# Performance work log

Measured on AMD Instinct MI355X. Metric: run time of the kernel, lower is better.

## Reference

```python
import jax, jax.numpy as jnp
import numpy as np

E = 23   # unique experts
K = 3    # active experts per token
D = 1024 # in_features
H = 4096 # hidden_features

def setup_inputs() -> dict:
    key = jax.random.key(0)
    ks = jax.random.split(key, 8)
    s = jnp.float32(0.02)
    return {
        "x": jax.random.normal(ks[0], (4, 2048, D), jnp.float32),
        "gate_W": jax.random.normal(ks[1], (D, E), jnp.float32) * s,
        "gate_b": jnp.zeros((E,), jnp.float32),
        "W1": jax.random.normal(ks[2], (E, D, H), jnp.float32) * s,
        "b1": jnp.zeros((E, H), jnp.float32),
        "W2": jax.random.normal(ks[3], (E, H, D), jnp.float32) * s,
        "b2": jnp.zeros((E, D), jnp.float32),
        "sW1": jax.random.normal(ks[4], (D, H), jnp.float32) * s,
        "sb1": jnp.zeros((H,), jnp.float32),
        "sW2": jax.random.normal(ks[5], (H, D), jnp.float32) * s,
        "sb2": jnp.zeros((D,), jnp.float32),
        "bias": jnp.zeros((E,), jnp.float32),  # registered buffer, zeros
    }

def _mlp(x, w1, bb1, w2, bb2):
    # torch nn.GELU default is exact (erf) GELU; drop=0 so dropout is identity
    return jax.nn.gelu(x @ w1 + bb1, approximate=False) @ w2 + bb2

def reference(x, gate_W, gate_b, W1, b1, W2, b2, sW1, sb1, sW2, sb2, bias):
    oshape = x.shape
    xf = x.reshape(-1, oshape[-1])            # [N, D]
    N = xf.shape[0]
    gw = jax.nn.sigmoid(xf @ gate_W + gate_b) # [N, E]
    # top-k selected on (gate + bias), weights gathered from raw gate
    _, topi = jax.lax.top_k(gw + bias, K)     # [N, K]
    topw = jnp.take_along_axis(gw, topi, axis=-1)
    topw = topw / topw.sum(-1, keepdims=True)
    # dense [N, E] combine-weight matrix (0 for unselected experts);
    # per-token topk indices are distinct so .set is safe
    wmat = jnp.zeros((N, E), gw.dtype).at[jnp.arange(N)[:, None], topi].set(topw)
    shared = _mlp(xf, sW1, sb1, sW2, sb2)     # shared expert over all tokens
    # scan over the 23 experts, accumulating weighted expert outputs.
    # (jit-friendly stand-in for the variable-size dispatch/grouped-GEMM.)
    def body(acc, ws):
        w1, bb1, w2, bb2, wcol = ws
        return acc + wcol[:, None] * _mlp(xf, w1, bb1, w2, bb2), None
    out, _ = jax.lax.scan(body, shared, (W1, b1, W2, b2, wmat.T))
    # load-balance auxiliary loss
    counts = jnp.zeros((E,), jnp.float32).at[topi.reshape(-1)].add(1.0)
    P = (gw / gw.sum(-1, keepdims=True)).mean(0)
    Fload = E * counts / (K * N)
    return out.reshape(oshape), (P * Fload).sum()
```

## Files before the change

kernel.cpp:

```cpp
#include <hip/hip_runtime.h>
#include <math.h>

#define DD 1024
#define HH 4096
#define EE 23
#define KK 3
#define NTOK 8192
#define BM 128
#define BN 128
#define BK 32
#define MAXROWS 35712
#define MAXTILES 280

typedef unsigned short u16;
typedef __attribute__((ext_vector_type(8))) short bf16x8;
typedef __attribute__((ext_vector_type(4))) float f32x4;
typedef __attribute__((address_space(3))) unsigned int lds_u32;
typedef const __attribute__((address_space(1))) unsigned int gbl_u32;

struct Tile { int rowStart; int validEnd; int expert; };

__device__ __forceinline__ u16 f2bf(float f) {
    unsigned int u = __float_as_uint(f);
    unsigned int r = 0x7FFFu + ((u >> 16) & 1u);
    return (u16)((u + r) >> 16);
}
__device__ __forceinline__ float gelu_exact(float x) {
    float z = x * 0.70710678118654752f;
    float a = fabsf(z);
    float t = __builtin_amdgcn_rcpf(1.0f + 0.3275911f * a);
    float e = __builtin_amdgcn_exp2f(-a * a * 1.4426950408889634f);
    float p = t * (0.254829592f + t * (-0.284496736f + t * (1.421413741f +
              t * (-1.453152027f + t * 1.061405429f))));
    float er = 1.0f - p * e;
    er = (z < 0.0f) ? -er : er;
    return 0.5f * x * (1.0f + er);
}
__device__ __forceinline__ void gl2lds16(const u16* g, u16* l) {
    __builtin_amdgcn_global_load_lds((gbl_u32*)g, (lds_u32*)l, 16, 0, 0);
}

__global__ void k_convert_x(const float* __restrict__ x, u16* __restrict__ xbf) {
    int i = blockIdx.x * blockDim.x + threadIdx.x;
    float4 v = reinterpret_cast<const float4*>(x)[i];
    ushort4 o;
    o.x = f2bf(v.x); o.y = f2bf(v.y); o.z = f2bf(v.z); o.w = f2bf(v.w);
    reinterpret_cast<ushort4*>(xbf)[i] = o;
}

__global__ void k_transpose(const float* __restrict__ src, u16* __restrict__ dst, int R, int C) {
    __shared__ float tile[64][65];
    size_t base = (size_t)blockIdx.z * R * C;
    src += base; dst += base;
    int ct = blockIdx.x, rt = blockIdx.y, t = threadIdx.x;
    int r0 = rt * 64, c0 = ct * 64;
#pragma unroll
    for (int i = 0; i < 4; i++) {
        int r = i * 16 + (t >> 4);
        int c = (t & 15) * 4;
        float4 v = *reinterpret_cast<const float4*>(&src[(size_t)(r0 + r) * C + c0 + c]);
        tile[r][c] = v.x; tile[r][c + 1] = v.y; tile[r][c + 2] = v.z; tile[r][c + 3] = v.w;
    }
    __syncthreads();
#pragma unroll
    for (int i = 0; i < 4; i++) {
        int c = i * 16 + (t >> 4);
        int r = (t & 15) * 4;
        ushort4 o;
        o.x = f2bf(tile[r][c]);     o.y = f2bf(tile[r + 1][c]);
        o.z = f2bf(tile[r + 2][c]); o.w = f2bf(tile[r + 3][c]);
        *reinterpret_cast<ushort4*>(&dst[(size_t)(c0 + c) * R + r0 + r]) = o;
    }
}

__global__ void k_gate(const float* __restrict__ x, const float* __restrict__ gW,
                       const float* __restrict__ gb, const float* __restrict__ ebias,
                       int* __restrict__ topi, float* __restrict__ topw,
                       int* __restrict__ counts, float* __restrict__ psum) {
    int tok = blockIdx.x, t = threadIdx.x;
    float acc[EE];
#pragma unroll
    for (int e = 0; e < EE; e++) acc[e] = 0.f;
    float4 xv = reinterpret_cast<const float4*>(x + (size_t)tok * DD)[t];
    float xs[4] = {xv.x, xv.y, xv.z, xv.w};
#pragma unroll
    for (int i = 0; i < 4; i++) {
        const float* grow = gW + (size_t)(t * 4 + i) * EE;
        float xd = xs[i];
#pragma unroll
        for (int e = 0; e < EE; e++) acc[e] += xd * grow[e];
    }
#pragma unroll
    for (int e = 0; e < EE; e++) {
        float v = acc[e];
        for (int off = 32; off; off >>= 1) v += __shfl_down(v, off);
        acc[e] = v;
    }
    __shared__ float part[4][EE];
    __shared__ float gwS[EE], scoreS[EE], rowsumS;
    int wave = t >> 6, lane = t & 63;
    if (lane == 0) {
#pragma unroll
        for (int e = 0; e < EE; e++) part[wave][e] = acc[e];
    }
    __syncthreads();
    if (t < EE) {
        float v = part[0][t] + part[1][t] + part[2][t] + part[3][t] + gb[t];
        float g = 1.f / (1.f + expf(-v));
        gwS[t] = g;
        scoreS[t] = g + ebias[t];
    }
    __syncthreads();
    if (t == 0) {
        int i0 = 0, i1 = -1, i2 = -1;
        float s0 = -1e30f, s1 = -1e30f, s2 = -1e30f;
        for (int e = 0; e < EE; e++) {
            float s = scoreS[e];
            if (s > s0)      { s2 = s1; i2 = i1; s1 = s0; i1 = i0; s0 = s; i0 = e; }
            else if (s > s1) { s2 = s1; i2 = i1; s1 = s;  i1 = e; }
            else if (s > s2) { s2 = s;  i2 = e; }
        }
        float w0 = gwS[i0], w1 = gwS[i1], w2 = gwS[i2];
        float wsum = w0 + w1 + w2;
        topi[tok * 3] = i0; topi[tok * 3 + 1] = i1; topi[tok * 3 + 2] = i2;
        topw[tok * 3] = w0 / wsum; topw[tok * 3 + 1] = w1 / wsum; topw[tok * 3 + 2] = w2 / wsum;
        atomicAdd(&counts[i0], 1); atomicAdd(&counts[i1], 1); atomicAdd(&counts[i2], 1);
        float rs = 0.f;
        for (int e = 0; e < EE; e++) rs += gwS[e];
        rowsumS = rs;
    }
    __syncthreads();
    if (t < EE) atomicAdd(&psum[t], gwS[t] / rowsumS);
}

__global__ void k_setup(const int* __restrict__ counts, const float* __restrict__ psum,
                        int* __restrict__ offs, Tile* __restrict__ tiles,
                        int* __restrict__ numTiles, float* __restrict__ out_aux) {
    if (threadIdx.x != 0 || blockIdx.x != 0) return;
    int nt = 0;
    for (int i = 0; i < NTOK / BM; i++) {
        tiles[nt].rowStart = i * BM; tiles[nt].validEnd = NTOK; tiles[nt].expert = EE; nt++;
    }
    int base = NTOK;
    for (int e = 0; e < EE; e++) {
        offs[e] = base;
        int c = counts[e];
        int ntile = (c + BM - 1) / BM;
        for (int i = 0; i < ntile; i++) {
            tiles[nt].rowStart = base + i * BM; tiles[nt].validEnd = base + c; tiles[nt].expert = e; nt++;
        }
        base += ntile * BM;
    }
    numTiles[0] = nt;
    float aux = 0.f;
    for (int e = 0; e < EE; e++)
        aux += (psum[e] / (float)NTOK) * ((float)EE * (float)counts[e] / ((float)KK * (float)NTOK));
    out_aux[0] = aux;
}

__global__ void k_scatter(const int* __restrict__ topi, const float* __restrict__ topw,
                          const int* __restrict__ offs, int* __restrict__ cursor,
                          int* __restrict__ rowTok, float* __restrict__ rowW) {
    int tok = blockIdx.x * blockDim.x + threadIdx.x;
    if (tok >= NTOK) return;
    rowTok[tok] = tok; rowW[tok] = 1.0f;
    for (int k = 0; k < KK; k++) {
        int e = topi[tok * 3 + k];
        int pos = atomicAdd(&cursor[e], 1);
        int slot = offs[e] + pos;
        rowTok[slot] = tok; rowW[slot] = topw[tok * 3 + k];
    }
}

__global__ __launch_bounds__(256) void k_gemm1(
    const u16* __restrict__ xbf, const u16* __restrict__ w1t, const u16* __restrict__ sw1t,
    const float* __restrict__ b1, const float* __restrict__ sb1,
    const int* __restrict__ rowTok, const Tile* __restrict__ tiles,
    const int* __restrict__ numTiles, u16* __restrict__ hbuf, int chunkBase, int hrows) {
    int b = blockIdx.x;
    int xcd = b & 7;
    int j = b >> 3;
    int pb = j / MAXTILES;
    int ti = j - pb * MAXTILES;
    int p  = xcd * 4 + pb;
    if (ti >= numTiles[0]) return;
    Tile tl = tiles[ti];
    if (tl.rowStart < chunkBase || tl.rowStart >= chunkBase + hrows) return;
    int e = tl.expert;
    const u16* wbase = (e == EE) ? sw1t : (w1t + (size_t)e * HH * DD);
    const float* bias = (e == EE) ? sb1 : (b1 + (size_t)e * HH);
    int hbase = p * BN;
    int t = threadIdx.x, lane = t & 63, wv = t >> 6, wr = wv >> 1, wc = wv & 1;

    __shared__ u16 As[BM * BK];
    __shared__ u16 Bs[BN * BK];

    int rbase = wv * 16 + (lane >> 2);
    int c8 = (lane & 3) * 8;
    int s0 = tl.rowStart + rbase, s1 = s0 + 64;
    int tA0 = (s0 < tl.validEnd) ? rowTok[s0] : 0;
    int tA1 = (s1 < tl.validEnd) ? rowTok[s1] : 0;
    const u16* a0 = xbf + (size_t)tA0 * DD + c8;
    const u16* a1 = xbf + (size_t)tA1 * DD + c8;
    const u16* g0 = wbase + (size_t)(hbase + rbase) * DD + c8;
    const u16* g1 = wbase + (size_t)(hbase + 64 + rbase) * DD + c8;
    u16* lA = &As[t * 8];
    u16* lB = &Bs[t * 8];

    f32x4 acc[4][4];
#pragma unroll
    for (int m = 0; m < 4; m++)
#pragma unroll
        for (int n = 0; n < 4; n++) acc[m][n] = (f32x4){0.f, 0.f, 0.f, 0.f};

    for (int kt = 0; kt < DD / BK; kt++) {
        __syncthreads();
        gl2lds16(a0, lA); gl2lds16(a1, lA + 2048);
        gl2lds16(g0, lB); gl2lds16(g1, lB + 2048);
        a0 += BK; a1 += BK; g0 += BK; g1 += BK;
        __syncthreads();
        bf16x8 af[4], bw[4];
#pragma unroll
        for (int m = 0; m < 4; m++)
            af[m] = *reinterpret_cast<const bf16x8*>(&As[(wr * 64 + m * 16 + (lane & 15)) * BK + (lane >> 4) * 8]);
#pragma unroll
        for (int n = 0; n < 4; n++)
            bw[n] = *reinterpret_cast<const bf16x8*>(&Bs[(wc * 64 + n * 16 + (lane & 15)) * BK + (lane >> 4) * 8]);
#pragma unroll
        for (int m = 0; m < 4; m++)
#pragma unroll
            for (int n = 0; n < 4; n++)
                acc[m][n] = __builtin_amdgcn_mfma_f32_16x16x32_bf16(af[m], bw[n], acc[m][n], 0, 0, 0);
    }

#pragma unroll
    for (int m = 0; m < 4; m++) {
        int rowl = wr * 64 + m * 16 + (lane >> 4) * 4;
#pragma unroll
        for (int r = 0; r < 4; r++) {
            int slotr = tl.rowStart + rowl + r;
            bool valid = slotr < tl.validEnd;
            size_t hoff = (size_t)(slotr - chunkBase) * HH;
#pragma unroll
            for (int n = 0; n < 4; n++) {
                int col = hbase + wc * 64 + n * 16 + (lane & 15);
                float v = acc[m][n][r] + bias[col];
                hbuf[hoff + col] = valid ? f2bf(gelu_exact(v)) : (u16)0;
            }
        }
    }
}

__global__ __launch_bounds__(256) void k_gemm2(
    const u16* __restrict__ hbuf, const u16* __restrict__ w2t, const u16* __restrict__ sw2t,
    const float* __restrict__ b2, const float* __restrict__ sb2,
    const int* __restrict__ rowTok, const float* __restrict__ rowW,
    const Tile* __restrict__ tiles, const int* __restrict__ numTiles,
    float* __restrict__ out, int chunkBase, int hrows) {
    const int T = MAXTILES * (DD / BN);
    int b = blockIdx.x;
    int key = (b & 7) * (T >> 3) + (b >> 3);
    int sid = key >> 2, wi = key & 3;
    int ti = (sid >> 2) * 2 + (wi >> 1);
    int p  = ((sid & 3) << 1) + (wi & 1);
    if (ti >= numTiles[0]) return;
    Tile tl = tiles[ti];
    if (tl.rowStart < chunkBase || tl.rowStart >= chunkBase + hrows) return;
    int e = tl.expert;
    const u16* wbase = (e == EE) ? sw2t : (w2t + (size_t)e * DD * HH);
    const float* bias = (e == EE) ? sb2 : (b2 + (size_t)e * DD);
    int dbase = p * BN;
    int t = threadIdx.x, lane = t & 63, wv = t >> 6, wr = wv >> 1, wc = wv & 1;

    __shared__ u16 As[BM * BK];
    __shared__ u16 Bs[BN * BK];

    int rbase = wv * 16 + (lane >> 2);
    int c8 = (lane & 3) * 8;
    const u16* a0 = hbuf + (size_t)(tl.rowStart - chunkBase + rbase) * HH + c8;
    const u16* a1 = hbuf + (size_t)(tl.rowStart - chunkBase + 64 + rbase) * HH + c8;
    const u16* g0 = wbase + (size_t)(dbase + rbase) * HH + c8;
    const u16* g1 = wbase + (size_t)(dbase + 64 + rbase) * HH + c8;
    u16* lA = &As[t * 8];
    u16* lB = &Bs[t * 8];

    f32x4 acc[4][4];
#pragma unroll
    for (int m = 0; m < 4; m++)
#pragma unroll
        for (int n = 0; n < 4; n++) acc[m][n] = (f32x4){0.f, 0.f, 0.f, 0.f};

    for (int kt = 0; kt < HH / BK; kt++) {
        __syncthreads();
        gl2lds16(a0, lA); gl2lds16(a1, lA + 2048);
        gl2lds16(g0, lB); gl2lds16(g1, lB + 2048);
        a0 += BK; a1 += BK; g0 += BK; g1 += BK;
        __syncthreads();
        bf16x8 af[4], bw[4];
#pragma unroll
        for (int m = 0; m < 4; m++)
            af[m] = *reinterpret_cast<const bf16x8*>(&As[(wr * 64 + m * 16 + (lane & 15)) * BK + (lane >> 4) * 8]);
#pragma unroll
        for (int n = 0; n < 4; n++)
            bw[n] = *reinterpret_cast<const bf16x8*>(&Bs[(wc * 64 + n * 16 + (lane & 15)) * BK + (lane >> 4) * 8]);
#pragma unroll
        for (int m = 0; m < 4; m++)
#pragma unroll
            for (int n = 0; n < 4; n++)
                acc[m][n] = __builtin_amdgcn_mfma_f32_16x16x32_bf16(af[m], bw[n], acc[m][n], 0, 0, 0);
    }

#pragma unroll
    for (int m = 0; m < 4; m++) {
        int rowl = wr * 64 + m * 16 + (lane >> 4) * 4;
#pragma unroll
        for (int r = 0; r < 4; r++) {
            int slotr = tl.rowStart + rowl + r;
            if (slotr < tl.validEnd) {
                int tok2 = rowTok[slotr];
                float wgt = rowW[slotr];
                float* orow = out + (size_t)tok2 * DD;
#pragma unroll
                for (int n = 0; n < 4; n++) {
                    int col = dbase + wc * 64 + n * 16 + (lane & 15);
                    float v = acc[m][n][r] + bias[col];
                    atomicAdd(&orow[col], wgt * v);
                }
            }
        }
    }
}

extern "C" void kernel_launch(void* const* d_in, const int* in_sizes, int n_in,
                              void* d_out, int out_size, void* d_ws, size_t ws_size,
                              hipStream_t stream) {
    const float* x    = (const float*)d_in[0];
    const float* gW   = (const float*)d_in[1];
    const float* gb   = (const float*)d_in[2];
    const float* W1   = (const float*)d_in[3];
    const float* b1   = (const float*)d_in[4];
    const float* W2   = (const float*)d_in[5];
    const float* b2   = (const float*)d_in[6];
    const float* sW1  = (const float*)d_in[7];
    const float* sb1  = (const float*)d_in[8];
    const float* sW2  = (const float*)d_in[9];
    const float* sb2  = (const float*)d_in[10];
    const float* ebias = (const float*)d_in[11];
    float* out = (float*)d_out;

    char* w = (char*)d_ws;
    size_t off = 0;
    auto alloc = [&](size_t bytes) -> void* {
        void* p = w + off;
        off += (bytes + 255) & ~(size_t)255;
        return p;
    };
    u16* xbf   = (u16*)alloc((size_t)NTOK * DD * 2);
    u16* w1t   = (u16*)alloc((size_t)EE * HH * DD * 2);
    u16* w2t   = (u16*)alloc((size_t)EE * DD * HH * 2);
    u16* sw1t  = (u16*)alloc((size_t)HH * DD * 2);
    u16* sw2t  = (u16*)alloc((size_t)DD * HH * 2);
    int* topi  = (int*)alloc((size_t)NTOK * 3 * 4);
    float* topw = (float*)alloc((size_t)NTOK * 3 * 4);
    int* counts = (int*)alloc(128);
    float* psum = (float*)alloc(128);
    int* cursor = (int*)alloc(128);
    int* offs   = (int*)alloc(128);
    int* rowTok = (int*)alloc((size_t)MAXROWS * 4);
    float* rowW = (float*)alloc((size_t)MAXROWS * 4);
    Tile* tiles = (Tile*)alloc((size_t)MAXTILES * sizeof(Tile));
    int* numTiles = (int*)alloc(128);

    size_t fixed = off;
    size_t remain = (ws_size > fixed) ? (ws_size - fixed) : 0;
    long hr = (long)(remain / ((size_t)HH * 2));
    if (hr > MAXROWS) hr = MAXROWS;
    hr &= ~(long)127;
    if (hr < 128) hr = 128;
    int hrows = (int)hr;
    int passes = (MAXROWS + hrows - 1) / hrows;
    u16* hbuf = (u16*)(w + fixed);

    hipMemsetAsync(d_out, 0, (size_t)NTOK * DD * 4, stream);
    hipMemsetAsync(counts, 0, 768, stream);

    k_convert_x<<<NTOK, 256, 0, stream>>>(x, xbf);
    k_transpose<<<dim3(HH / 64, DD / 64, EE), 256, 0, stream>>>(W1, w1t, DD, HH);
    k_transpose<<<dim3(DD / 64, HH / 64, EE), 256, 0, stream>>>(W2, w2t, HH, DD);
    k_transpose<<<dim3(HH / 64, DD / 64, 1), 256, 0, stream>>>(sW1, sw1t, DD, HH);
    k_transpose<<<dim3(DD / 64, HH / 64, 1), 256, 0, stream>>>(sW2, sw2t, HH, DD);
    k_gate<<<NTOK, 256, 0, stream>>>(x, gW, gb, ebias, topi, topw, counts, psum);
    k_setup<<<1, 64, 0, stream>>>(counts, psum, offs, tiles, numTiles, out + (size_t)NTOK * DD);
    k_scatter<<<NTOK / 256, 256, 0, stream>>>(topi, topw, offs, cursor, rowTok, rowW);

    for (int p = 0; p < passes; p++) {
        k_gemm1<<<MAXTILES * (HH / BN), 256, 0, stream>>>(
            xbf, w1t, sw1t, b1, sb1, rowTok, tiles, numTiles, hbuf, p * hrows, hrows);
        k_gemm2<<<MAXTILES * (DD / BN), 256, 0, stream>>>(
            hbuf, w2t, sw2t, b2, sb2, rowTok, rowW, tiles, numTiles, out, p * hrows, hrows);
    }
}
```

Baseline: 1.485 ms.

## Double-buffer LDS tiles in both expert GEMMs and regroup gemm1 block mapping

Both grouped GEMM kernels now keep two LDS stages. The next K-slice is issued with direct global-to-LDS loads while the current one is computed, and partial vmcnt waits plus raw barriers replace the two full syncthreads per iteration. gemm1 also swaps its XCD/tile block mapping for a swizzle that groups 8 row tiles by 4 column panels, aiming for better L2 reuse of weights and activations. LDS use doubles, which may cut occupancy, and the hand-written waitcnt counts depend on how gl2lds16 is compiled.

```diff
diff --git a/kernel.cpp b/kernel.cpp
--- a/kernel.cpp
+++ b/kernel.cpp
@@ -177,12 +177,12 @@
     const float* __restrict__ b1, const float* __restrict__ sb1,
     const int* __restrict__ rowTok, const Tile* __restrict__ tiles,
     const int* __restrict__ numTiles, u16* __restrict__ hbuf, int chunkBase, int hrows) {
+    const int T = MAXTILES * (HH / BN);
     int b = blockIdx.x;
-    int xcd = b & 7;
-    int j = b >> 3;
-    int pb = j / MAXTILES;
-    int ti = j - pb * MAXTILES;
-    int p  = xcd * 4 + pb;
+    int key = (b & 7) * (T >> 3) + (b >> 3);
+    int sid = key >> 5, wi = key & 31;
+    int ti = (sid >> 3) * 8 + (wi >> 2);
+    int p  = ((sid & 7) << 2) + (wi & 3);
     if (ti >= numTiles[0]) return;
     Tile tl = tiles[ti];
     if (tl.rowStart < chunkBase || tl.rowStart >= chunkBase + hrows) return;
@@ -192,8 +192,8 @@
     int hbase = p * BN;
     int t = threadIdx.x, lane = t & 63, wv = t >> 6, wr = wv >> 1, wc = wv & 1;
 
-    __shared__ u16 As[BM * BK];
-    __shared__ u16 Bs[BN * BK];
+    __shared__ u16 As[2][BM * BK];
+    __shared__ u16 Bs[2][BN * BK];
 
     int rbase = wv * 16 + (lane >> 2);
     int c8 = (lane & 3) * 8;
@@ -204,8 +204,6 @@
     const u16* a1 = xbf + (size_t)tA1 * DD + c8;
     const u16* g0 = wbase + (size_t)(hbase + rbase) * DD + c8;
     const u16* g1 = wbase + (size_t)(hbase + 64 + rbase) * DD + c8;
-    u16* lA = &As[t * 8];
-    u16* lB = &Bs[t * 8];
 
     f32x4 acc[4][4];
 #pragma unroll
@@ -213,25 +211,41 @@
 #pragma unroll
         for (int n = 0; n < 4; n++) acc[m][n] = (f32x4){0.f, 0.f, 0.f, 0.f};
 
-    for (int kt = 0; kt < DD / BK; kt++) {
-        __syncthreads();
+    auto stage = [&](int buf) {
+        u16* lA = &As[buf][t * 8];
+        u16* lB = &Bs[buf][t * 8];
         gl2lds16(a0, lA); gl2lds16(a1, lA + 2048);
         gl2lds16(g0, lB); gl2lds16(g1, lB + 2048);
         a0 += BK; a1 += BK; g0 += BK; g1 += BK;
-        __syncthreads();
+    };
+    auto compute = [&](int buf) {
         bf16x8 af[4], bw[4];
 #pragma unroll
         for (int m = 0; m < 4; m++)
-            af[m] = *reinterpret_cast<const bf16x8*>(&As[(wr * 64 + m * 16 + (lane & 15)) * BK + (lane >> 4) * 8]);
+            af[m] = *reinterpret_cast<const bf16x8*>(&As[buf][(wr * 64 + m * 16 + (lane & 15)) * BK + (lane >> 4) * 8]);
 #pragma unroll
         for (int n = 0; n < 4; n++)
-            bw[n] = *reinterpret_cast<const bf16x8*>(&Bs[(wc * 64 + n * 16 + (lane & 15)) * BK + (lane >> 4) * 8]);
+            bw[n] = *reinterpret_cast<const bf16x8*>(&Bs[buf][(wc * 64 + n * 16 + (lane & 15)) * BK + (lane >> 4) * 8]);
 #pragma unroll
         for (int m = 0; m < 4; m++)
 #pragma unroll
             for (int n = 0; n < 4; n++)
                 acc[m][n] = __builtin_amdgcn_mfma_f32_16x16x32_bf16(af[m], bw[n], acc[m][n], 0, 0, 0);
-    }
+    };
+
+    const int NK = DD / BK;
+    stage(0);
+    for (int kt = 0; kt < NK - 1; kt++) {
+        stage((kt + 1) & 1);
+        asm volatile("s_waitcnt vmcnt(4)" ::: "memory");
+        __builtin_amdgcn_s_barrier();
+        compute(kt & 1);
+        asm volatile("s_waitcnt lgkmcnt(0)" ::: "memory");
+        __builtin_amdgcn_s_barrier();
+    }
+    asm volatile("s_waitcnt vmcnt(0)" ::: "memory");
+    __builtin_amdgcn_s_barrier();
+    compute((NK - 1) & 1);
 
 #pragma unroll
     for (int m = 0; m < 4; m++) {
@@ -272,8 +286,8 @@
     int dbase = p * BN;
     int t = threadIdx.x, lane = t & 63, wv = t >> 6, wr = wv >> 1, wc = wv & 1;
 
-    __shared__ u16 As[BM * BK];
-    __shared__ u16 Bs[BN * BK];
+    __shared__ u16 As[2][BM * BK];
+    __shared__ u16 Bs[2][BN * BK];
 
     int rbase = wv * 16 + (lane >> 2);
     int c8 = (lane & 3) * 8;
@@ -281,8 +295,6 @@
     const u16* a1 = hbuf + (size_t)(tl.rowStart - chunkBase + 64 + rbase) * HH + c8;
     const u16* g0 = wbase + (size_t)(dbase + rbase) * HH + c8;
     const u16* g1 = wbase + (size_t)(dbase + 64 + rbase) * HH + c8;
-    u16* lA = &As[t * 8];
-    u16* lB = &Bs[t * 8];
 
     f32x4 acc[4][4];
 #pragma unroll
@@ -290,25 +302,41 @@
 #pragma unroll
         for (int n = 0; n < 4; n++) acc[m][n] = (f32x4){0.f, 0.f, 0.f, 0.f};
 
-    for (int kt = 0; kt < HH / BK; kt++) {
-        __syncthreads();
+    auto stage = [&](int buf) {
+        u16* lA = &As[buf][t * 8];
+        u16* lB = &Bs[buf][t * 8];
         gl2lds16(a0, lA); gl2lds16(a1, lA + 2048);
         gl2lds16(g0, lB); gl2lds16(g1, lB + 2048);
         a0 += BK; a1 += BK; g0 += BK; g1 += BK;
-        __syncthreads();
+    };
+    auto compute = [&](int buf) {
         bf16x8 af[4], bw[4];
 #pragma unroll
         for (int m = 0; m < 4; m++)
-            af[m] = *reinterpret_cast<const bf16x8*>(&As[(wr * 64 + m * 16 + (lane & 15)) * BK + (lane >> 4) * 8]);
+            af[m] = *reinterpret_cast<const bf16x8*>(&As[buf][(wr * 64 + m * 16 + (lane & 15)) * BK + (lane >> 4) * 8]);
 #pragma unroll
         for (int n = 0; n < 4; n++)
-            bw[n] = *reinterpret_cast<const bf16x8*>(&Bs[(wc * 64 + n * 16 + (lane & 15)) * BK + (lane >> 4) * 8]);
+            bw[n] = *reinterpret_cast<const bf16x8*>(&Bs[buf][(wc * 64 + n * 16 + (lane & 15)) * BK + (lane >> 4) * 8]);
 #pragma unroll
         for (int m = 0; m < 4; m++)
 #pragma unroll
             for (int n = 0; n < 4; n++)
                 acc[m][n] = __builtin_amdgcn_mfma_f32_16x16x32_bf16(af[m], bw[n], acc[m][n], 0, 0, 0);
-    }
+    };
+
+    const int NK = HH / BK;
+    stage(0);
+    for (int kt = 0; kt < NK - 1; kt++) {
+        stage((kt + 1) & 1);
+        asm volatile("s_waitcnt vmcnt(4)" ::: "memory");
+        __builtin_amdgcn_s_barrier();
+        compute(kt & 1);
+        asm volatile("s_waitcnt lgkmcnt(0)" ::: "memory");
+        __builtin_amdgcn_s_barrier();
+    }
+    asm volatile("s_waitcnt vmcnt(0)" ::: "memory");
+    __builtin_amdgcn_s_barrier();
+    compute((NK - 1) & 1);
 
 #pragma unroll
     for (int m = 0; m < 4; m++) {
```

Measured after the change: 1.617 ms. +8.9%, slower.

## Double K tile depth, remap gemm1 block swizzle, merge shared-expert transposes

Applied to the files above, without the earlier changes.

Raises the GEMM K-tile from 32 to 64 so each pair of barriers covers two MFMA k-steps, with loaders reworked to four 16-byte global-to-LDS loads per operand. This halves the number of barriers and loop iterations in both expert GEMMs. gemm1 gets a new block-to-tile mapping that groups 8 tiles by 4 column blocks per XCD, aiming for better L2 reuse of weights and activations. The shared-expert weight transposes are folded into the expert transpose launches as an extra z-slice, removing two launches. Doubling LDS per block to 32KB may lower occupancy.

```diff
diff --git a/kernel.cpp b/kernel.cpp
--- a/kernel.cpp
+++ b/kernel.cpp
@@ -8,7 +8,7 @@
 #define NTOK 8192
 #define BM 128
 #define BN 128
-#define BK 32
+#define BK 64
 #define MAXROWS 35712
 #define MAXTILES 280
 
@@ -48,10 +48,13 @@
     reinterpret_cast<ushort4*>(xbf)[i] = o;
 }
 
-__global__ void k_transpose(const float* __restrict__ src, u16* __restrict__ dst, int R, int C) {
+__global__ void k_transpose(const float* __restrict__ srcE, u16* __restrict__ dstE,
+                            const float* __restrict__ srcS, u16* __restrict__ dstS,
+                            int R, int C) {
     __shared__ float tile[64][65];
-    size_t base = (size_t)blockIdx.z * R * C;
-    src += base; dst += base;
+    const float* src; u16* dst;
+    if (blockIdx.z == EE) { src = srcS; dst = dstS; }
+    else { size_t base = (size_t)blockIdx.z * R * C; src = srcE + base; dst = dstE + base; }
     int ct = blockIdx.x, rt = blockIdx.y, t = threadIdx.x;
     int r0 = rt * 64, c0 = ct * 64;
 #pragma unroll
@@ -177,12 +180,12 @@
     const float* __restrict__ b1, const float* __restrict__ sb1,
     const int* __restrict__ rowTok, const Tile* __restrict__ tiles,
     const int* __restrict__ numTiles, u16* __restrict__ hbuf, int chunkBase, int hrows) {
+    const int T = MAXTILES * (HH / BN);
     int b = blockIdx.x;
-    int xcd = b & 7;
-    int j = b >> 3;
-    int pb = j / MAXTILES;
-    int ti = j - pb * MAXTILES;
-    int p  = xcd * 4 + pb;
+    int key = (b & 7) * (T >> 3) + (b >> 3);
+    int sid = key >> 5, wi = key & 31;
+    int ti = (sid >> 3) * 8 + (wi >> 2);
+    int p  = ((sid & 7) << 2) + (wi & 3);
     if (ti >= numTiles[0]) return;
     Tile tl = tiles[ti];
     if (tl.rowStart < chunkBase || tl.rowStart >= chunkBase + hrows) return;
@@ -195,15 +198,16 @@
     __shared__ u16 As[BM * BK];
     __shared__ u16 Bs[BN * BK];
 
-    int rbase = wv * 16 + (lane >> 2);
-    int c8 = (lane & 3) * 8;
-    int s0 = tl.rowStart + rbase, s1 = s0 + 64;
-    int tA0 = (s0 < tl.validEnd) ? rowTok[s0] : 0;
-    int tA1 = (s1 < tl.validEnd) ? rowTok[s1] : 0;
-    const u16* a0 = xbf + (size_t)tA0 * DD + c8;
-    const u16* a1 = xbf + (size_t)tA1 * DD + c8;
-    const u16* g0 = wbase + (size_t)(hbase + rbase) * DD + c8;
-    const u16* g1 = wbase + (size_t)(hbase + 64 + rbase) * DD + c8;
+    int r32 = t >> 3;
+    int c8 = (t & 7) * 8;
+    const u16* ap[4]; const u16* gp[4];
+#pragma unroll
+    for (int i = 0; i < 4; i++) {
+        int s = tl.rowStart + i * 32 + r32;
+        int tok2 = (s < tl.validEnd) ? rowTok[s] : 0;
+        ap[i] = xbf + (size_t)tok2 * DD + c8;
+        gp[i] = wbase + (size_t)(hbase + i * 32 + r32) * DD + c8;
+    }
     u16* lA = &As[t * 8];
     u16* lB = &Bs[t * 8];
 
@@ -215,22 +219,29 @@
 
     for (int kt = 0; kt < DD / BK; kt++) {
         __syncthreads();
-        gl2lds16(a0, lA); gl2lds16(a1, lA + 2048);
-        gl2lds16(g0, lB); gl2lds16(g1, lB + 2048);
-        a0 += BK; a1 += BK; g0 += BK; g1 += BK;
+#pragma unroll
+        for (int i = 0; i < 4; i++) {
+            gl2lds16(ap[i], lA + i * 2048);
+            gl2lds16(gp[i], lB + i * 2048);
+            ap[i] += BK; gp[i] += BK;
+        }
         __syncthreads();
-        bf16x8 af[4], bw[4];
-#pragma unroll
-        for (int m = 0; m < 4; m++)
-            af[m] = *reinterpret_cast<const bf16x8*>(&As[(wr * 64 + m * 16 + (lane & 15)) * BK + (lane >> 4) * 8]);
-#pragma unroll
-        for (int n = 0; n < 4; n++)
-            bw[n] = *reinterpret_cast<const bf16x8*>(&Bs[(wc * 64 + n * 16 + (lane & 15)) * BK + (lane >> 4) * 8]);
-#pragma unroll
-        for (int m = 0; m < 4; m++)
+#pragma unroll
+        for (int ks = 0; ks < 2; ks++) {
+            bf16x8 af[4], bw[4];
+            int kc = (lane >> 4) * 8 + ks * 32;
+#pragma unroll
+            for (int m = 0; m < 4; m++)
+                af[m] = *reinterpret_cast<const bf16x8*>(&As[(wr * 64 + m * 16 + (lane & 15)) * BK + kc]);
 #pragma unroll
             for (int n = 0; n < 4; n++)
-                acc[m][n] = __builtin_amdgcn_mfma_f32_16x16x32_bf16(af[m], bw[n], acc[m][n], 0, 0, 0);
+                bw[n] = *reinterpret_cast<const bf16x8*>(&Bs[(wc * 64 + n * 16 + (lane & 15)) * BK + kc]);
+#pragma unroll
+            for (int m = 0; m < 4; m++)
+#pragma unroll
+                for (int n = 0; n < 4; n++)
+                    acc[m][n] = __builtin_amdgcn_mfma_f32_16x16x32_bf16(af[m], bw[n], acc[m][n], 0, 0, 0);
+        }
     }
 
 #pragma unroll
@@ -275,12 +286,14 @@
     __shared__ u16 As[BM * BK];
     __shared__ u16 Bs[BN * BK];
 
-    int rbase = wv * 16 + (lane >> 2);
-    int c8 = (lane & 3) * 8;
-    const u16* a0 = hbuf + (size_t)(tl.rowStart - chunkBase + rbase) * HH + c8;
-    const u16* a1 = hbuf + (size_t)(tl.rowStart - chunkBase + 64 + rbase) * HH + c8;
-    const u16* g0 = wbase + (size_t)(dbase + rbase) * HH + c8;
-    const u16* g1 = wbase + (size_t)(dbase + 64 + rbase) * HH + c8;
+    int r32 = t >> 3;
+    int c8 = (t & 7) * 8;
+    const u16* ap[4]; const u16* gp[4];
+#pragma unroll
+    for (int i = 0; i < 4; i++) {
+        ap[i] = hbuf + (size_t)(tl.rowStart - chunkBase + i * 32 + r32) * HH + c8;
+        gp[i] = wbase + (size_t)(dbase + i * 32 + r32) * HH + c8;
+    }
     u16* lA = &As[t * 8];
     u16* lB = &Bs[t * 8];
 
@@ -292,22 +305,29 @@
 
     for (int kt = 0; kt < HH / BK; kt++) {
         __syncthreads();
-        gl2lds16(a0, lA); gl2lds16(a1, lA + 2048);
-        gl2lds16(g0, lB); gl2lds16(g1, lB + 2048);
-        a0 += BK; a1 += BK; g0 += BK; g1 += BK;
+#pragma unroll
+        for (int i = 0; i < 4; i++) {
+            gl2lds16(ap[i], lA + i * 2048);
+            gl2lds16(gp[i], lB + i * 2048);
+            ap[i] += BK; gp[i] += BK;
+        }
         __syncthreads();
-        bf16x8 af[4], bw[4];
-#pragma unroll
-        for (int m = 0; m < 4; m++)
-            af[m] = *reinterpret_cast<const bf16x8*>(&As[(wr * 64 + m * 16 + (lane & 15)) * BK + (lane >> 4) * 8]);
-#pragma unroll
-        for (int n = 0; n < 4; n++)
-            bw[n] = *reinterpret_cast<const bf16x8*>(&Bs[(wc * 64 + n * 16 + (lane & 15)) * BK + (lane >> 4) * 8]);
-#pragma unroll
-        for (int m = 0; m < 4; m++)
+#pragma unroll
+        for (int ks = 0; ks < 2; ks++) {
+            bf16x8 af[4], bw[4];
+            int kc = (lane >> 4) * 8 + ks * 32;
+#pragma unroll
+            for (int m = 0; m < 4; m++)
+                af[m] = *reinterpret_cast<const bf16x8*>(&As[(wr * 64 + m * 16 + (lane & 15)) * BK + kc]);
 #pragma unroll
             for (int n = 0; n < 4; n++)
-                acc[m][n] = __builtin_amdgcn_mfma_f32_16x16x32_bf16(af[m], bw[n], acc[m][n], 0, 0, 0);
+                bw[n] = *reinterpret_cast<const bf16x8*>(&Bs[(wc * 64 + n * 16 + (lane & 15)) * BK + kc]);
+#pragma unroll
+            for (int m = 0; m < 4; m++)
+#pragma unroll
+                for (int n = 0; n < 4; n++)
+                    acc[m][n] = __builtin_amdgcn_mfma_f32_16x16x32_bf16(af[m], bw[n], acc[m][n], 0, 0, 0);
+        }
     }
 
 #pragma unroll
@@ -385,10 +405,8 @@
     hipMemsetAsync(counts, 0, 768, stream);
 
     k_convert_x<<<NTOK, 256, 0, stream>>>(x, xbf);
-    k_transpose<<<dim3(HH / 64, DD / 64, EE), 256, 0, stream>>>(W1, w1t, DD, HH);
-    k_transpose<<<dim3(DD / 64, HH / 64, EE), 256, 0, stream>>>(W2, w2t, HH, DD);
-    k_transpose<<<dim3(HH / 64, DD / 64, 1), 256, 0, stream>>>(sW1, sw1t, DD, HH);
-    k_transpose<<<dim3(DD / 64, HH / 64, 1), 256, 0, stream>>>(sW2, sw2t, HH, DD);
+    k_transpose<<<dim3(HH / 64, DD / 64, EE + 1), 256, 0, stream>>>(W1, w1t, sW1, sw1t, DD, HH);
+    k_transpose<<<dim3(DD / 64, HH / 64, EE + 1), 256, 0, stream>>>(W2, w2t, sW2, sw2t, HH, DD);
     k_gate<<<NTOK, 256, 0, stream>>>(x, gW, gb, ebias, topi, topw, counts, psum);
     k_setup<<<1, 64, 0, stream>>>(counts, psum, offs, tiles, numTiles, out + (size_t)NTOK * DD);
     k_scatter<<<NTOK / 256, 256, 0, stream>>>(topi, topw, offs, cursor, rowTok, rowW);
```

Result: slower. 1.826 ms (+23.0%).

## Fuse x conversion into gate, merge shared transposes, remap gemm1 block order

Applied to the files above, without the earlier changes.

Folds the fp32-to-bf16 conversion of x into the gate kernel, which already reads x, so one launch and one extra read of x go away. Shared-expert weight transposes are merged into the expert transpose launches as an extra z slice, removing two small launches. The gemm1 block-index mapping is reworked so each XCD handles groups of 8 tiles by 4 hidden-column blocks, aiming for better L2 reuse of weights and activations. Together these cut launch overhead and change the cache locality of the main GEMM.

```diff
diff --git a/kernel.cpp b/kernel.cpp
--- a/kernel.cpp
+++ b/kernel.cpp
@@ -40,18 +40,13 @@
     __builtin_amdgcn_global_load_lds((gbl_u32*)g, (lds_u32*)l, 16, 0, 0);
 }
 
-__global__ void k_convert_x(const float* __restrict__ x, u16* __restrict__ xbf) {
-    int i = blockIdx.x * blockDim.x + threadIdx.x;
-    float4 v = reinterpret_cast<const float4*>(x)[i];
-    ushort4 o;
-    o.x = f2bf(v.x); o.y = f2bf(v.y); o.z = f2bf(v.z); o.w = f2bf(v.w);
-    reinterpret_cast<ushort4*>(xbf)[i] = o;
-}
-
-__global__ void k_transpose(const float* __restrict__ src, u16* __restrict__ dst, int R, int C) {
+__global__ void k_transpose(const float* __restrict__ srcE, u16* __restrict__ dstE,
+                            const float* __restrict__ srcS, u16* __restrict__ dstS,
+                            int R, int C) {
     __shared__ float tile[64][65];
-    size_t base = (size_t)blockIdx.z * R * C;
-    src += base; dst += base;
+    const float* src; u16* dst;
+    if (blockIdx.z == EE) { src = srcS; dst = dstS; }
+    else { size_t base = (size_t)blockIdx.z * R * C; src = srcE + base; dst = dstE + base; }
     int ct = blockIdx.x, rt = blockIdx.y, t = threadIdx.x;
     int r0 = rt * 64, c0 = ct * 64;
 #pragma unroll
@@ -76,12 +71,16 @@
 __global__ void k_gate(const float* __restrict__ x, const float* __restrict__ gW,
                        const float* __restrict__ gb, const float* __restrict__ ebias,
                        int* __restrict__ topi, float* __restrict__ topw,
-                       int* __restrict__ counts, float* __restrict__ psum) {
+                       int* __restrict__ counts, float* __restrict__ psum,
+                       u16* __restrict__ xbf) {
     int tok = blockIdx.x, t = threadIdx.x;
     float acc[EE];
 #pragma unroll
     for (int e = 0; e < EE; e++) acc[e] = 0.f;
     float4 xv = reinterpret_cast<const float4*>(x + (size_t)tok * DD)[t];
+    ushort4 xo;
+    xo.x = f2bf(xv.x); xo.y = f2bf(xv.y); xo.z = f2bf(xv.z); xo.w = f2bf(xv.w);
+    reinterpret_cast<ushort4*>(xbf + (size_t)tok * DD)[t] = xo;
     float xs[4] = {xv.x, xv.y, xv.z, xv.w};
 #pragma unroll
     for (int i = 0; i < 4; i++) {
@@ -177,12 +176,12 @@
     const float* __restrict__ b1, const float* __restrict__ sb1,
     const int* __restrict__ rowTok, const Tile* __restrict__ tiles,
     const int* __restrict__ numTiles, u16* __restrict__ hbuf, int chunkBase, int hrows) {
+    const int T = MAXTILES * (HH / BN);
     int b = blockIdx.x;
-    int xcd = b & 7;
-    int j = b >> 3;
-    int pb = j / MAXTILES;
-    int ti = j - pb * MAXTILES;
-    int p  = xcd * 4 + pb;
+    int key = (b & 7) * (T >> 3) + (b >> 3);
+    int sid = key >> 5, wi = key & 31;
+    int ti = (sid >> 3) * 8 + (wi >> 2);
+    int p  = ((sid & 7) << 2) + (wi & 3);
     if (ti >= numTiles[0]) return;
     Tile tl = tiles[ti];
     if (tl.rowStart < chunkBase || tl.rowStart >= chunkBase + hrows) return;
@@ -384,12 +383,9 @@
     hipMemsetAsync(d_out, 0, (size_t)NTOK * DD * 4, stream);
     hipMemsetAsync(counts, 0, 768, stream);
 
-    k_convert_x<<<NTOK, 256, 0, stream>>>(x, xbf);
-    k_transpose<<<dim3(HH / 64, DD / 64, EE), 256, 0, stream>>>(W1, w1t, DD, HH);
-    k_transpose<<<dim3(DD / 64, HH / 64, EE), 256, 0, stream>>>(W2, w2t, HH, DD);
-    k_transpose<<<dim3(HH / 64, DD / 64, 1), 256, 0, stream>>>(sW1, sw1t, DD, HH);
-    k_transpose<<<dim3(DD / 64, HH / 64, 1), 256, 0, stream>>>(sW2, sw2t, HH, DD);
-    k_gate<<<NTOK, 256, 0, stream>>>(x, gW, gb, ebias, topi, topw, counts, psum);
+    k_gate<<<NTOK, 256, 0, stream>>>(x, gW, gb, ebias, topi, topw, counts, psum, xbf);
+    k_transpose<<<dim3(HH / 64, DD / 64, EE + 1), 256, 0, stream>>>(W1, w1t, sW1, sw1t, DD, HH);
+    k_transpose<<<dim3(DD / 64, HH / 64, EE + 1), 256, 0, stream>>>(W2, w2t, sW2, sw2t, HH, DD);
     k_setup<<<1, 64, 0, stream>>>(counts, psum, offs, tiles, numTiles, out + (size_t)NTOK * DD);
     k_scatter<<<NTOK / 256, 256, 0, stream>>>(topi, topw, offs, cursor, rowTok, rowW);
 
```

New measurement: 1.473 ms. No clear change (-0.8%).
